# Kernel tuning notes

Measured on AMD Instinct MI355X. Metric: run time of the kernel, lower is better.

## Reference

```python
import jax, jax.numpy as jnp
import numpy as np
from jax.ops import segment_sum

N_USERS = 100_000
N_ITEMS = 200_000
D = 64
NNZ = 5_000_000
GNN_LAYERS = 2


def setup_inputs() -> dict:
    key = jax.random.key(0)
    k0, k1, k2, k3, k4 = jax.random.split(key, 5)
    # Embedding tables (xavier-ish scale)
    user_emb = jax.random.normal(k0, (N_USERS, D), jnp.float32) * 0.1
    item_emb = jax.random.normal(k1, (N_ITEMS, D), jnp.float32) * 0.1
    # Sparse normalized bipartite adjacency adj_norm [n_users, n_items] in COO form
    adj_vals = jax.random.uniform(k2, (NNZ,), jnp.float32)
    adj_rows = jax.random.randint(k3, (NNZ,), 0, N_USERS, jnp.int32)
    adj_cols = jax.random.randint(k4, (NNZ,), 0, N_ITEMS, jnp.int32)
    return {
        "user_emb": user_emb,
        "item_emb": item_emb,
        "adj_vals": adj_vals,
        "adj_rows": adj_rows,
        "adj_cols": adj_cols,
    }


def reference(user_emb, item_emb, adj_vals, adj_rows, adj_cols):
    """Student_LightGCL.forward with is_test=True.

    NormLayer with mode 'None' is identity. Then gnn_layer rounds of
    bipartite sparse propagation:
      Z_u = adj_norm   @ E_i   (spmm -> gather + segment_sum over users)
      Z_i = adj_norm.T @ E_u
    Output: mean over layer-0..L embeddings for users and items.
    """
    E_u, E_i = user_emb, item_emb
    sum_u, sum_i = E_u, E_i
    for _ in range(GNN_LAYERS):
        # Z_u[r] = sum_{e: rows[e]==r} vals[e] * E_i[cols[e]]
        Z_u = segment_sum(adj_vals[:, None] * E_i[adj_cols], adj_rows,
                          num_segments=N_USERS)
        Z_i = segment_sum(adj_vals[:, None] * E_u[adj_rows], adj_cols,
                          num_segments=N_ITEMS)
        E_u, E_i = Z_u, Z_i
        sum_u = sum_u + E_u
        sum_i = sum_i + E_i
    inv = 1.0 / (GNN_LAYERS + 1)
    return sum_u * inv, sum_i * inv
```

## Files before the change

kernel.cpp:

```cpp
#include <hip/hip_runtime.h>


constexpr int D = 64;
constexpr int RPB = 64;
constexpr int ACC = 32;
constexpr int NBMAX = 5120;
constexpr int REF_CAP = 4000;
constexpr int PASSB_EDGES = 8192;

static __device__ __forceinline__ unsigned short f32_to_bf16(float f) {
    unsigned u = __float_as_uint(f);
    unsigned r = u + 0x7FFFu + ((u >> 16) & 1u);
    return (unsigned short)(r >> 16);
}
static __device__ __forceinline__ float bf16_lo(unsigned g) {
    return __uint_as_float(g << 16);
}
static __device__ __forceinline__ float bf16_hi(unsigned g) {
    return __uint_as_float(g & 0xFFFF0000u);
}


__global__ __launch_bounds__(1024) void bucket_hist(
    const int* __restrict__ rows, const int* __restrict__ cols,
    int* __restrict__ bktCnt, int nu, int nnz, int NB) {
    __shared__ int cnt[NBMAX];
    for (int i = threadIdx.x; i < NB; i += blockDim.x) cnt[i] = 0;
    __syncthreads();
    int stride = gridDim.x * blockDim.x;
    for (int e = blockIdx.x * blockDim.x + threadIdx.x; e < nnz; e += stride) {
        atomicAdd(&cnt[rows[e] >> 6], 1);
        atomicAdd(&cnt[(nu + cols[e]) >> 6], 1);
    }
    __syncthreads();
    for (int i = threadIdx.x; i < NB; i += blockDim.x)
        if (cnt[i]) atomicAdd(&bktCnt[i], cnt[i]);
}

__global__ void scan_buckets(const int* __restrict__ bktCnt,
                             int* __restrict__ bktBase, int* __restrict__ bktCur,
                             int NB, int total) {
    __shared__ int tsum[256];
    int t = threadIdx.x;
    const int IT = (NB + 255) / 256;
    int v[20];
    int s = 0;
    for (int k = 0; k < IT; k++) {
        int i = t * IT + k;
        v[k] = (i < NB) ? bktCnt[i] : 0;
        s += v[k];
    }
    tsum[t] = s;
    __syncthreads();
    for (int off = 1; off < 256; off <<= 1) {
        int x = (t >= off) ? tsum[t - off] : 0;
        __syncthreads();
        tsum[t] += x;
        __syncthreads();
    }
    int excl = (t > 0) ? tsum[t - 1] : 0;
    for (int k = 0; k < IT; k++) {
        int i = t * IT + k;
        if (i < NB) { bktBase[i] = excl; bktCur[i] = excl; excl += v[k]; }
    }
    if (t == 255) bktBase[NB] = total;
}

__global__ __launch_bounds__(1024) void pass_bucket(
    const float* __restrict__ vals, const int* __restrict__ rows,
    const int* __restrict__ cols, int* __restrict__ bktCur,
    int2* __restrict__ tmp, int nu, int nnz, int NB) {
    __shared__ int cnt[NBMAX];
    for (int i = threadIdx.x; i < NB; i += 1024) cnt[i] = 0;
    __syncthreads();
    int base = blockIdx.x * PASSB_EDGES;
    for (int k = 0; k < PASSB_EDGES / 1024; k++) {
        int e = base + k * 1024 + threadIdx.x;
        if (e < nnz) {
            atomicAdd(&cnt[rows[e] >> 6], 1);
            atomicAdd(&cnt[(nu + cols[e]) >> 6], 1);
        }
    }
    __syncthreads();
    for (int i = threadIdx.x; i < NB; i += 1024) {
        int c = cnt[i];
        if (c) cnt[i] = atomicAdd(&bktCur[i], c);
    }
    __syncthreads();
    for (int k = 0; k < PASSB_EDGES / 1024; k++) {
        int e = base + k * 1024 + threadIdx.x;
        if (e < nnz) {
            int r = rows[e], c = cols[e];
            int iv = __float_as_int(vals[e]);
            int gi = nu + c;
            int p1 = atomicAdd(&cnt[r >> 6], 1);
            tmp[p1] = make_int2(((r & 63) << 19) | gi, iv);
            int p2 = atomicAdd(&cnt[gi >> 6], 1);
            tmp[p2] = make_int2(((gi & 63) << 19) | r, iv);
        }
    }
}

__global__ void convert_e0(const float* __restrict__ Eu,
                           const float* __restrict__ Ei,
                           unsigned short* __restrict__ Ecat,
                           long long nuD, long long nD) {
    long long stride = (long long)gridDim.x * blockDim.x * 4;
    for (long long i = ((long long)blockIdx.x * blockDim.x + threadIdx.x) * 4;
         i < nD; i += stride) {
        const float* src = (i < nuD) ? (Eu + i) : (Ei + (i - nuD));
        float4 f = *(const float4*)src;
        unsigned short o0 = f32_to_bf16(f.x), o1 = f32_to_bf16(f.y);
        unsigned short o2 = f32_to_bf16(f.z), o3 = f32_to_bf16(f.w);
        *(uint2*)(Ecat + i) =
            make_uint2(((unsigned)o1 << 16) | o0, ((unsigned)o3 << 16) | o2);
    }
}

__global__ __launch_bounds__(512) void accum_sort_l1(
    int2* __restrict__ tmp, const int* __restrict__ bktBase,
    int* __restrict__ rowStart,
    const unsigned short* __restrict__ gsrc,
    unsigned short* __restrict__ Zout,
    int nu, int nR) {
    __shared__ int2 stage[REF_CAP];
    __shared__ unsigned short idx[REF_CAP];
    __shared__ int h[RPB], cur[RPB], rs[RPB + 1];
    int b = blockIdx.x;
    int beg = bktBase[b], end = bktBase[b + 1];
    int n = end - beg;
    int t = threadIdx.x;
    if (t < RPB) h[t] = 0;
    if (t == 0) { stage[0] = make_int2(0, 0); idx[0] = 0; }
    __syncthreads();

    int w = t >> 6, lane = t & 63;
    int q = lane >> 4, m = lane & 15;
    const uint2* gp = (const uint2*)gsrc + m;

    if (n <= REF_CAP) {
        for (int e = t; e < n; e += 512) {
            int2 v = tmp[beg + e];
            stage[e] = v;
            atomicAdd(&h[(v.x >> 19) & (RPB - 1)], 1);
        }
        __syncthreads();
        int myc = (t < RPB) ? h[t] : 0;
        for (int off = 1; off < RPB; off <<= 1) {
            int x = 0;
            if (t < RPB && t >= off) x = h[t - off];
            __syncthreads();
            if (t < RPB) h[t] += x;
            __syncthreads();
        }
        if (t < RPB) {
            int excl = h[t] - myc;
            cur[t] = excl;
            rs[t] = excl;
            rowStart[(size_t)b * RPB + t] = beg + excl;
        }
        if (t == 0) rs[RPB] = n;
        __syncthreads();
        for (int e = t; e < n; e += 512) {
            int2 v = stage[e];
            int p = atomicAdd(&cur[(v.x >> 19) & (RPB - 1)], 1);
            idx[p] = (unsigned short)e;
        }
        __syncthreads();
        for (int e = t; e < n; e += 512) tmp[beg + e] = stage[idx[e]];

        for (int k = 0; k < 8; k += 2) {
            int rlA = (w << 3) + k;
            int grA = b * RPB + rlA;
            if (grA >= nR) break;
            bool hasB = (grA + 1) < nR;
            int eA0 = rs[rlA], eA1 = rs[rlA + 1];
            int eB0 = eA1;
            int eB1 = hasB ? rs[rlA + 2] : eA1;
            int nA = eA1 - eA0, nB = eB1 - eB0;
            int iters = ((nA > nB ? nA : nB) + 3) >> 2;

            float a0 = 0.f, a1 = 0.f, a2 = 0.f, a3 = 0.f;
            float b0 = 0.f, b1 = 0.f, b2 = 0.f, b3 = 0.f;
            int eA = eA0 + q, eB = eB0 + q;

            bool okA = eA < eA1, okB = eB < eB1;
            int2 sA = stage[idx[okA ? eA : 0]];
            int2 sB = stage[idx[okB ? eB : 0]];
            uint2 gA = gp[(okA ? (sA.x & 0x7FFFF) : 0) << 4];
            uint2 gB = gp[(okB ? (sB.x & 0x7FFFF) : 0) << 4];
            float vA = okA ? __int_as_float(sA.y) : 0.f;
            float vB = okB ? __int_as_float(sB.y) : 0.f;

            for (int i = 0; i < iters; i++) {
                bool okA1 = (eA + 4) < eA1, okB1 = (eB + 4) < eB1;
                int2 sAn = stage[idx[okA1 ? eA + 4 : 0]];
                int2 sBn = stage[idx[okB1 ? eB + 4 : 0]];

                a0 += vA * bf16_lo(gA.x); a1 += vA * bf16_hi(gA.x);
                a2 += vA * bf16_lo(gA.y); a3 += vA * bf16_hi(gA.y);
                b0 += vB * bf16_lo(gB.x); b1 += vB * bf16_hi(gB.x);
                b2 += vB * bf16_lo(gB.y); b3 += vB * bf16_hi(gB.y);

                gA = gp[(okA1 ? (sAn.x & 0x7FFFF) : 0) << 4];
                gB = gp[(okB1 ? (sBn.x & 0x7FFFF) : 0) << 4];
                vA = okA1 ? __int_as_float(sAn.y) : 0.f;
                vB = okB1 ? __int_as_float(sBn.y) : 0.f;
                eA += 4; eB += 4;
            }

            a0 += __shfl_xor(a0, 16, 64); a0 += __shfl_xor(a0, 32, 64);
            a1 += __shfl_xor(a1, 16, 64); a1 += __shfl_xor(a1, 32, 64);
            a2 += __shfl_xor(a2, 16, 64); a2 += __shfl_xor(a2, 32, 64);
            a3 += __shfl_xor(a3, 16, 64); a3 += __shfl_xor(a3, 32, 64);
            b0 += __shfl_xor(b0, 16, 64); b0 += __shfl_xor(b0, 32, 64);
            b1 += __shfl_xor(b1, 16, 64); b1 += __shfl_xor(b1, 32, 64);
            b2 += __shfl_xor(b2, 16, 64); b2 += __shfl_xor(b2, 32, 64);
            b3 += __shfl_xor(b3, 16, 64); b3 += __shfl_xor(b3, 32, 64);

            int wr = (q == 0) ? grA : ((q == 1 && hasB) ? grA + 1 : -1);
            if (wr >= 0) {
                float r0 = (q == 0) ? a0 : b0;
                float r1 = (q == 0) ? a1 : b1;
                float r2 = (q == 0) ? a2 : b2;
                float r3 = (q == 0) ? a3 : b3;
                long long o = (long long)wr * D + m * 4;
                unsigned p0 = ((unsigned)f32_to_bf16(r1) << 16) | f32_to_bf16(r0);
                unsigned p1 = ((unsigned)f32_to_bf16(r3) << 16) | f32_to_bf16(r2);
                *(uint2*)(Zout + o) = make_uint2(p0, p1);
            }
        }
    } else {
        if (t < RPB) rowStart[(size_t)b * RPB + t] = (t == 0) ? -(beg + 1) : 0;
        __syncthreads();
        for (int k = 0; k < 8; k += 2) {
            int rlA = (w << 3) + k;
            int grA = b * RPB + rlA;
            if (grA >= nR) break;
            bool hasB = (grA + 1) < nR;
            float a0 = 0.f, a1 = 0.f, a2 = 0.f, a3 = 0.f;
            float b0 = 0.f, b1 = 0.f, b2 = 0.f, b3 = 0.f;
            int iters = (n + 3) >> 2;
            int e = beg + q;
            for (int i = 0; i < iters; i++) {
                int2 s = (e < end) ? tmp[e] : make_int2(0, 0);
                int rl = (s.x >> 19) & (RPB - 1);
                bool okA = (e < end) && (rl == rlA);
                bool okB = (e < end) && hasB && (rl == rlA + 1);
                int rx = (okA | okB) ? (s.x & 0x7FFFF) : 0;
                float vA = okA ? __int_as_float(s.y) : 0.f;
                float vB = okB ? __int_as_float(s.y) : 0.f;
                uint2 g = gp[rx << 4];
                a0 += vA * bf16_lo(g.x); a1 += vA * bf16_hi(g.x);
                a2 += vA * bf16_lo(g.y); a3 += vA * bf16_hi(g.y);
                b0 += vB * bf16_lo(g.x); b1 += vB * bf16_hi(g.x);
                b2 += vB * bf16_lo(g.y); b3 += vB * bf16_hi(g.y);
                e += 4;
            }
            a0 += __shfl_xor(a0, 16, 64); a0 += __shfl_xor(a0, 32, 64);
            a1 += __shfl_xor(a1, 16, 64); a1 += __shfl_xor(a1, 32, 64);
            a2 += __shfl_xor(a2, 16, 64); a2 += __shfl_xor(a2, 32, 64);
            a3 += __shfl_xor(a3, 16, 64); a3 += __shfl_xor(a3, 32, 64);
            b0 += __shfl_xor(b0, 16, 64); b0 += __shfl_xor(b0, 32, 64);
            b1 += __shfl_xor(b1, 16, 64); b1 += __shfl_xor(b1, 32, 64);
            b2 += __shfl_xor(b2, 16, 64); b2 += __shfl_xor(b2, 32, 64);
            b3 += __shfl_xor(b3, 16, 64); b3 += __shfl_xor(b3, 32, 64);
            int wr = (q == 0) ? grA : ((q == 1 && hasB) ? grA + 1 : -1);
            if (wr >= 0) {
                float r0 = (q == 0) ? a0 : b0;
                float r1 = (q == 0) ? a1 : b1;
                float r2 = (q == 0) ? a2 : b2;
                float r3 = (q == 0) ? a3 : b3;
                long long o = (long long)wr * D + m * 4;
                unsigned p0 = ((unsigned)f32_to_bf16(r1) << 16) | f32_to_bf16(r0);
                unsigned p1 = ((unsigned)f32_to_bf16(r3) << 16) | f32_to_bf16(r2);
                *(uint2*)(Zout + o) = make_uint2(p0, p1);
            }
        }
    }
}

__global__ __launch_bounds__(256, 8) void accum7_kernel(
    const int2* __restrict__ tmp, const int* __restrict__ bktBase,
    const int* __restrict__ rowStart,
    const unsigned short* __restrict__ gsrc,
    const float* __restrict__ Eu0, const float* __restrict__ Ei0,
    const unsigned short* __restrict__ Z1,
    float* __restrict__ out,
    int nu, int nR) {
    int b = blockIdx.x;
    int w = threadIdx.x >> 6, lane = threadIdx.x & 63;
    int q = lane >> 4, m = lane & 15;
    int rb64 = (b * ACC) >> 6;
    int bEnd = bktBase[rb64 + 1];
    int rb0 = rowStart[(size_t)rb64 << 6];
    bool sorted = (rb0 >= 0);
    const uint2* gp = (const uint2*)gsrc + m;

    for (int k = 0; k < 8; k += 2) {
        int grA = b * ACC + (w << 3) + k;
        if (grA >= nR) break;
        bool hasB = (grA + 1) < nR;

        float a0 = 0.f, a1 = 0.f, a2 = 0.f, a3 = 0.f;
        float b0 = 0.f, b1 = 0.f, b2 = 0.f, b3 = 0.f;

        if (sorted) {
            int eA0 = rowStart[grA], eA1 = rowStart[grA + 1];
            int eB0 = eA1;
            int eB1 = hasB ? (((grA & 63) == 62) ? bEnd : rowStart[grA + 2])
                           : eB0;
            int nA = eA1 - eA0, nB = eB1 - eB0;
            int iters = ((nA > nB ? nA : nB) + 3) >> 2;
            int eA = eA0 + q, eB = eB0 + q;

            int2 sAc = tmp[eA], sBc = tmp[eB];
            int2 sAn = tmp[eA + 4], sBn = tmp[eB + 4];
            bool okA = eA < eA1, okB = eB < eB1;
            uint2 gAc = gp[(okA ? (sAc.x & 0x7FFFF) : 0) << 4];
            uint2 gBc = gp[(okB ? (sBc.x & 0x7FFFF) : 0) << 4];
            float vAc = okA ? __int_as_float(sAc.y) : 0.f;
            float vBc = okB ? __int_as_float(sBc.y) : 0.f;

            for (int i = 0; i < iters; i++) {
                int2 sAn2 = tmp[eA + 8];
                int2 sBn2 = tmp[eB + 8];
                bool okA1 = (eA + 4) < eA1;
                bool okB1 = (eB + 4) < eB1;
                uint2 gAn = gp[(okA1 ? (sAn.x & 0x7FFFF) : 0) << 4];
                uint2 gBn = gp[(okB1 ? (sBn.x & 0x7FFFF) : 0) << 4];
                float vAn = okA1 ? __int_as_float(sAn.y) : 0.f;
                float vBn = okB1 ? __int_as_float(sBn.y) : 0.f;

                a0 += vAc * bf16_lo(gAc.x); a1 += vAc * bf16_hi(gAc.x);
                a2 += vAc * bf16_lo(gAc.y); a3 += vAc * bf16_hi(gAc.y);
                b0 += vBc * bf16_lo(gBc.x); b1 += vBc * bf16_hi(gBc.x);
                b2 += vBc * bf16_lo(gBc.y); b3 += vBc * bf16_hi(gBc.y);

                sAn = sAn2; sBn = sBn2;
                gAc = gAn;  gBc = gBn;
                vAc = vAn;  vBc = vBn;
                eA += 4; eB += 4;
            }
        } else {
            int beg = -(rb0 + 1);
            int n = bEnd - beg;
            int iters = (n + 3) >> 2;
            int e = beg + q;
            int rlA = grA & 63;
            for (int i = 0; i < iters; i++) {
                int2 s = tmp[e];
                int rl = (s.x >> 19) & 63;
                bool in = e < bEnd;
                bool okA = in && (rl == rlA);
                bool okB = in && hasB && (rl == rlA + 1);
                int rx = (okA | okB) ? (s.x & 0x7FFFF) : 0;
                float vA = okA ? __int_as_float(s.y) : 0.f;
                float vB = okB ? __int_as_float(s.y) : 0.f;
                uint2 g = gp[rx << 4];
                a0 += vA * bf16_lo(g.x); a1 += vA * bf16_hi(g.x);
                a2 += vA * bf16_lo(g.y); a3 += vA * bf16_hi(g.y);
                b0 += vB * bf16_lo(g.x); b1 += vB * bf16_hi(g.x);
                b2 += vB * bf16_lo(g.y); b3 += vB * bf16_hi(g.y);
                e += 4;
            }
        }

        a0 += __shfl_xor(a0, 16, 64); a0 += __shfl_xor(a0, 32, 64);
        a1 += __shfl_xor(a1, 16, 64); a1 += __shfl_xor(a1, 32, 64);
        a2 += __shfl_xor(a2, 16, 64); a2 += __shfl_xor(a2, 32, 64);
        a3 += __shfl_xor(a3, 16, 64); a3 += __shfl_xor(a3, 32, 64);
        b0 += __shfl_xor(b0, 16, 64); b0 += __shfl_xor(b0, 32, 64);
        b1 += __shfl_xor(b1, 16, 64); b1 += __shfl_xor(b1, 32, 64);
        b2 += __shfl_xor(b2, 16, 64); b2 += __shfl_xor(b2, 32, 64);
        b3 += __shfl_xor(b3, 16, 64); b3 += __shfl_xor(b3, 32, 64);

        int wr = (q == 0) ? grA : ((q == 1 && hasB) ? grA + 1 : -1);
        if (wr >= 0) {
            float r0 = (q == 0) ? a0 : b0;
            float r1 = (q == 0) ? a1 : b1;
            float r2 = (q == 0) ? a2 : b2;
            float r3 = (q == 0) ? a3 : b3;
            long long o = (long long)wr * D + m * 4;
            const float* e0p = (wr < nu)
                ? (Eu0 + o) : (Ei0 + o - (long long)nu * D);
            float4 e0 = *(const float4*)e0p;
            uint2 z = *(const uint2*)(Z1 + o);
            const float inv3 = 1.f / 3.f;
            float4 ov;
            ov.x = (e0.x + bf16_lo(z.x) + r0) * inv3;
            ov.y = (e0.y + bf16_hi(z.x) + r1) * inv3;
            ov.z = (e0.z + bf16_lo(z.y) + r2) * inv3;
            ov.w = (e0.w + bf16_hi(z.y) + r3) * inv3;
            *(float4*)(out + o) = ov;
        }
    }
}


__global__ void spmm_edge(const float* __restrict__ vals,
                          const int* __restrict__ rows,
                          const int* __restrict__ cols,
                          const float* __restrict__ Eu,
                          const float* __restrict__ Ei,
                          float* __restrict__ Zu, float* __restrict__ Zi,
                          float scale, int nnz) {
    long long gid = (long long)blockIdx.x * blockDim.x + threadIdx.x;
    if (gid >= (long long)nnz * D) return;
    int e = (int)(gid >> 6);
    int d = (int)(gid & 63);
    float v = vals[e] * scale;
    long long r = rows[e];
    long long c = cols[e];
    atomicAdd(&Zu[r * D + d], v * Ei[c * D + d]);
    atomicAdd(&Zi[c * D + d], v * Eu[r * D + d]);
}

__global__ void combine_kernel(const float* __restrict__ E0,
                               const float* __restrict__ Z1,
                               float* __restrict__ out, long long n4) {
    long long i = (long long)blockIdx.x * blockDim.x + threadIdx.x;
    if (i >= n4) return;
    const float4 a = reinterpret_cast<const float4*>(E0)[i];
    const float4 b = reinterpret_cast<const float4*>(Z1)[i];
    const float inv3 = 1.0f / 3.0f;
    float4 o;
    o.x = (a.x + b.x) * inv3;
    o.y = (a.y + b.y) * inv3;
    o.z = (a.z + b.z) * inv3;
    o.w = (a.w + b.w) * inv3;
    reinterpret_cast<float4*>(out)[i] = o;
}


static inline size_t align256(size_t x) { return (x + 255) & ~(size_t)255; }

extern "C" void kernel_launch(void* const* d_in, const int* in_sizes, int n_in,
                              void* d_out, int out_size, void* d_ws, size_t ws_size,
                              hipStream_t stream) {
    const float* user_emb = (const float*)d_in[0];
    const float* item_emb = (const float*)d_in[1];
    const float* vals     = (const float*)d_in[2];
    const int*   rows     = (const int*)d_in[3];
    const int*   cols     = (const int*)d_in[4];

    const int nu  = in_sizes[0] / D;
    const int ni  = in_sizes[1] / D;
    const int nnz = in_sizes[2];
    const int nR  = nu + ni;
    const int NB  = (nR + RPB - 1) / RPB;

    float* out = (float*)d_out;

    size_t off = 0;
    size_t o_tmp  = off; off += align256(((size_t)2 * nnz + 32) * sizeof(int2));
    size_t o_E    = off; off += align256((size_t)nR * D * sizeof(unsigned short));
    size_t o_Z1   = off; off += align256((size_t)nR * D * sizeof(unsigned short));
    size_t o_cnt  = off; off += align256((size_t)(NB + 1) * sizeof(int));
    size_t o_base = off; off += align256((size_t)(NB + 2) * sizeof(int));
    size_t o_cur  = off; off += align256((size_t)(NB + 1) * sizeof(int));
    size_t o_row  = off; off += align256(((size_t)NB * RPB + 1) * sizeof(int));
    size_t needed = off;

    bool fits19 = (nR < (1 << 19));

    if (ws_size >= needed && NB <= NBMAX && fits19) {
        char* w = (char*)d_ws;
        int2*           tmp      = (int2*)(w + o_tmp);
        unsigned short* Ecat     = (unsigned short*)(w + o_E);
        unsigned short* Z1bf     = (unsigned short*)(w + o_Z1);
        int*            bktCnt   = (int*)(w + o_cnt);
        int*            bktBase  = (int*)(w + o_base);
        int*            bktCur   = (int*)(w + o_cur);
        int*            rowStart = (int*)(w + o_row);

        hipMemsetAsync(bktCnt, 0, (size_t)NB * sizeof(int), stream);

        bucket_hist<<<512, 1024, 0, stream>>>(rows, cols, bktCnt, nu, nnz, NB);
        scan_buckets<<<1, 256, 0, stream>>>(bktCnt, bktBase, bktCur, NB, 2 * nnz);

        unsigned gB = (unsigned)((nnz + PASSB_EDGES - 1) / PASSB_EDGES);
        pass_bucket<<<gB, 1024, 0, stream>>>(vals, rows, cols, bktCur, tmp,
                                             nu, nnz, NB);

        long long nD = (long long)nR * D;
        long long nuD = (long long)nu * D;
        unsigned gC = (unsigned)((nD / 4 + 255) / 256);
        if (gC > 4096) gC = 4096;
        convert_e0<<<gC, 256, 0, stream>>>(user_emb, item_emb, Ecat, nuD, nD);

        accum_sort_l1<<<NB, 512, 0, stream>>>(tmp, bktBase, rowStart, Ecat,
                                              Z1bf, nu, nR);

        unsigned gA = (unsigned)((nR + ACC - 1) / ACC);
        accum7_kernel<<<gA, 256, 0, stream>>>(
            tmp, bktBase, rowStart, Z1bf, user_emb, item_emb, Z1bf,
            out, nu, nR);
    } else {
        float* Zu1 = (float*)d_ws;
        float* Zi1 = Zu1 + (size_t)nu * D;
        float* out_u = out;
        float* out_i = out + (size_t)nu * D;
        hipMemsetAsync(d_ws, 0, (size_t)nR * D * sizeof(float), stream);

        const int threads = 256;
        long long tot = (long long)nnz * D;
        unsigned blocks = (unsigned)((tot + threads - 1) / threads);

        spmm_edge<<<blocks, threads, 0, stream>>>(vals, rows, cols, user_emb,
                                                  item_emb, Zu1, Zi1, 1.0f, nnz);
        long long nu4 = (long long)nu * D / 4;
        long long ni4 = (long long)ni * D / 4;
        combine_kernel<<<(unsigned)((nu4 + 255) / 256), 256, 0, stream>>>(
            user_emb, Zu1, out_u, nu4);
        combine_kernel<<<(unsigned)((ni4 + 255) / 256), 256, 0, stream>>>(
            item_emb, Zi1, out_i, ni4);
        spmm_edge<<<blocks, threads, 0, stream>>>(vals, rows, cols, Zu1, Zi1,
                                                  out_u, out_i, 1.0f / 3.0f, nnz);
    }
}
```

Baseline: 704.7 us.

## Replace global-atomic bucket scatter with per-block count, column scan, and deterministic scatter

```diff
diff --git a/kernel.cpp b/kernel.cpp
--- a/kernel.cpp
+++ b/kernel.cpp
@@ -21,20 +21,43 @@
 }
 
 
-__global__ __launch_bounds__(1024) void bucket_hist(
+__global__ __launch_bounds__(1024) void count_kernel(
     const int* __restrict__ rows, const int* __restrict__ cols,
-    int* __restrict__ bktCnt, int nu, int nnz, int NB) {
+    unsigned short* __restrict__ cnts16, int nu, int nnz, int NB) {
     __shared__ int cnt[NBMAX];
-    for (int i = threadIdx.x; i < NB; i += blockDim.x) cnt[i] = 0;
-    __syncthreads();
-    int stride = gridDim.x * blockDim.x;
-    for (int e = blockIdx.x * blockDim.x + threadIdx.x; e < nnz; e += stride) {
-        atomicAdd(&cnt[rows[e] >> 6], 1);
-        atomicAdd(&cnt[(nu + cols[e]) >> 6], 1);
-    }
-    __syncthreads();
-    for (int i = threadIdx.x; i < NB; i += blockDim.x)
-        if (cnt[i]) atomicAdd(&bktCnt[i], cnt[i]);
+    for (int i = threadIdx.x; i < NB; i += 1024) cnt[i] = 0;
+    __syncthreads();
+    int base = blockIdx.x * PASSB_EDGES;
+    for (int k = 0; k < PASSB_EDGES / 1024; k++) {
+        int e = base + k * 1024 + threadIdx.x;
+        if (e < nnz) {
+            atomicAdd(&cnt[rows[e] >> 6], 1);
+            atomicAdd(&cnt[(nu + cols[e]) >> 6], 1);
+        }
+    }
+    __syncthreads();
+    for (int i = threadIdx.x; i < NB; i += 1024)
+        cnts16[(size_t)blockIdx.x * NB + i] = (unsigned short)cnt[i];
+}
+
+__global__ __launch_bounds__(64) void scanA_kernel(
+    const unsigned short* __restrict__ cnts16, int* __restrict__ offs,
+    int* __restrict__ totals, int NB, int NBLK) {
+    int b = blockIdx.x;
+    int lane = threadIdx.x;
+    int carry = 0;
+    for (int c0 = 0; c0 < NBLK; c0 += 64) {
+        int blk = c0 + lane;
+        int v = (blk < NBLK) ? (int)cnts16[(size_t)blk * NB + b] : 0;
+        int x = v;
+        for (int off = 1; off < 64; off <<= 1) {
+            int n = __shfl_up(x, off, 64);
+            if (lane >= off) x += n;
+        }
+        if (blk < NBLK) offs[(size_t)b * NBLK + blk] = carry + x - v;
+        carry += __shfl(x, 63, 64);
+    }
+    if (lane == 0) totals[b] = carry;
 }
 
 __global__ void scan_buckets(const int* __restrict__ bktCnt,
@@ -64,6 +87,47 @@
         if (i < NB) { bktBase[i] = excl; bktCur[i] = excl; excl += v[k]; }
     }
     if (t == 255) bktBase[NB] = total;
+}
+
+__global__ __launch_bounds__(1024) void passB_kernel(
+    const float* __restrict__ vals, const int* __restrict__ rows,
+    const int* __restrict__ cols, const int* __restrict__ bktBase,
+    const int* __restrict__ offs, int2* __restrict__ tmp,
+    int nu, int nnz, int NB, int NBLK) {
+    __shared__ int cur[NBMAX];
+    for (int i = threadIdx.x; i < NB; i += 1024)
+        cur[i] = bktBase[i] + offs[(size_t)i * NBLK + blockIdx.x];
+    __syncthreads();
+    int base = blockIdx.x * PASSB_EDGES;
+    for (int k = 0; k < PASSB_EDGES / 1024; k++) {
+        int e = base + k * 1024 + threadIdx.x;
+        if (e < nnz) {
+            int r = rows[e], c = cols[e];
+            int iv = __float_as_int(vals[e]);
+            int gi = nu + c;
+            int p1 = atomicAdd(&cur[r >> 6], 1);
+            tmp[p1] = make_int2(((r & 63) << 19) | gi, iv);
+            int p2 = atomicAdd(&cur[gi >> 6], 1);
+            tmp[p2] = make_int2(((gi & 63) << 19) | r, iv);
+        }
+    }
+}
+
+
+__global__ __launch_bounds__(1024) void bucket_hist(
+    const int* __restrict__ rows, const int* __restrict__ cols,
+    int* __restrict__ bktCnt, int nu, int nnz, int NB) {
+    __shared__ int cnt[NBMAX];
+    for (int i = threadIdx.x; i < NB; i += blockDim.x) cnt[i] = 0;
+    __syncthreads();
+    int stride = gridDim.x * blockDim.x;
+    for (int e = blockIdx.x * blockDim.x + threadIdx.x; e < nnz; e += stride) {
+        atomicAdd(&cnt[rows[e] >> 6], 1);
+        atomicAdd(&cnt[(nu + cols[e]) >> 6], 1);
+    }
+    __syncthreads();
+    for (int i = threadIdx.x; i < NB; i += blockDim.x)
+        if (cnt[i]) atomicAdd(&bktCnt[i], cnt[i]);
 }
 
 __global__ __launch_bounds__(1024) void pass_bucket(
@@ -449,6 +513,7 @@
     const int nnz = in_sizes[2];
     const int nR  = nu + ni;
     const int NB  = (nR + RPB - 1) / RPB;
+    const int NBLK = (nnz + PASSB_EDGES - 1) / PASSB_EDGES;
 
     float* out = (float*)d_out;
 
@@ -460,11 +525,14 @@
     size_t o_base = off; off += align256((size_t)(NB + 2) * sizeof(int));
     size_t o_cur  = off; off += align256((size_t)(NB + 1) * sizeof(int));
     size_t o_row  = off; off += align256(((size_t)NB * RPB + 1) * sizeof(int));
-    size_t needed = off;
+    size_t needed_mid = off;
+    size_t o_c16  = off; off += align256((size_t)NB * NBLK * sizeof(unsigned short));
+    size_t o_offs = off; off += align256((size_t)NB * NBLK * sizeof(int));
+    size_t needed_new = off;
 
     bool fits19 = (nR < (1 << 19));
 
-    if (ws_size >= needed && NB <= NBMAX && fits19) {
+    if (ws_size >= needed_mid && NB <= NBMAX && fits19) {
         char* w = (char*)d_ws;
         int2*           tmp      = (int2*)(w + o_tmp);
         unsigned short* Ecat     = (unsigned short*)(w + o_E);
@@ -474,14 +542,26 @@
         int*            bktCur   = (int*)(w + o_cur);
         int*            rowStart = (int*)(w + o_row);
 
-        hipMemsetAsync(bktCnt, 0, (size_t)NB * sizeof(int), stream);
-
-        bucket_hist<<<512, 1024, 0, stream>>>(rows, cols, bktCnt, nu, nnz, NB);
-        scan_buckets<<<1, 256, 0, stream>>>(bktCnt, bktBase, bktCur, NB, 2 * nnz);
-
-        unsigned gB = (unsigned)((nnz + PASSB_EDGES - 1) / PASSB_EDGES);
-        pass_bucket<<<gB, 1024, 0, stream>>>(vals, rows, cols, bktCur, tmp,
-                                             nu, nnz, NB);
+        if (ws_size >= needed_new) {
+            unsigned short* cnts16 = (unsigned short*)(w + o_c16);
+            int*            offs   = (int*)(w + o_offs);
+
+            count_kernel<<<NBLK, 1024, 0, stream>>>(rows, cols, cnts16,
+                                                    nu, nnz, NB);
+            scanA_kernel<<<NB, 64, 0, stream>>>(cnts16, offs, bktCnt, NB, NBLK);
+            scan_buckets<<<1, 256, 0, stream>>>(bktCnt, bktBase, bktCur,
+                                                NB, 2 * nnz);
+            passB_kernel<<<NBLK, 1024, 0, stream>>>(vals, rows, cols, bktBase,
+                                                    offs, tmp, nu, nnz, NB, NBLK);
+        } else {
+            hipMemsetAsync(bktCnt, 0, (size_t)NB * sizeof(int), stream);
+            bucket_hist<<<512, 1024, 0, stream>>>(rows, cols, bktCnt,
+                                                  nu, nnz, NB);
+            scan_buckets<<<1, 256, 0, stream>>>(bktCnt, bktBase, bktCur,
+                                                NB, 2 * nnz);
+            pass_bucket<<<NBLK, 1024, 0, stream>>>(vals, rows, cols, bktCur,
+                                                   tmp, nu, nnz, NB);
+        }
 
         long long nD = (long long)nR * D;
         long long nuD = (long long)nu * D;
```

Result: no change. 710.2 us (+0.8%).
